# Optimization experiments

Measured on AMD Instinct MI355X. Metric: run time of the kernel, lower is better.

## Reference

```python
import jax, jax.numpy as jnp
import numpy as np

B, N, D = 8, 4096, 2048
DL = 64
NCLS = 2


def setup_inputs() -> dict:
    key = jax.random.key(0)
    k_x, k_tn, k_v, k_w, k_fw, k_fb = jax.random.split(key, 6)
    x = jax.random.normal(k_x, (B, N, D), dtype=jnp.float32)
    # valid patch counts in [1, N] so no bag is fully masked
    true_num = jax.random.randint(k_tn, (B,), 1, N + 1, dtype=jnp.int32)
    std1 = 1.0 / np.sqrt(DL * D)
    V = jax.random.uniform(k_v, (D, DL), minval=-std1, maxval=std1, dtype=jnp.float32)
    std2 = 1.0 / np.sqrt(DL)
    W = jax.random.uniform(k_w, (DL, 1), minval=-std2, maxval=std2, dtype=jnp.float32)
    lim = 1.0 / np.sqrt(D)  # nn.Linear default init
    fc_w = jax.random.uniform(k_fw, (NCLS, D), minval=-lim, maxval=lim, dtype=jnp.float32)
    fc_b = jax.random.uniform(k_fb, (NCLS,), minval=-lim, maxval=lim, dtype=jnp.float32)
    return {"x": x, "true_num": true_num, "V": V, "W": W, "fc_w": fc_w, "fc_b": fc_b}


def reference(x, true_num, V, W, fc_w, fc_b):
    # MILAtten: attention scores over N patches
    x_ = jnp.tanh(jnp.einsum("bnd,dl->bnl", x, V))            # B x N x dl
    dis = jnp.einsum("bnl,lo->bn", x_, W) / np.sqrt(DL)        # B x N
    mask = jnp.arange(x.shape[1])[None, :] < true_num[:, None]  # B x N valid mask
    dis = jnp.where(mask, dis, jnp.float32(-1e20))
    soft_assign = jax.nn.softmax(dis, axis=1)                  # B x N
    feat_fusion = jnp.einsum("bn,bnd->bd", soft_assign, x)     # B x D
    # eval mode: dropout is identity
    logits = feat_fusion @ fc_w.T + fc_b                       # B x class_num
    cls_probs = jax.nn.softmax(logits, axis=1)
    return (cls_probs, soft_assign)
```

## Files before the change

kernel.cpp:

```cpp
#include <hip/hip_runtime.h>
#include <hip/hip_bf16.h>
#include <math.h>

#define BB 8
#define NN 4096
#define DD 2048
#define DLL 64
#define NCLS 2

typedef __attribute__((ext_vector_type(8))) short bf16x8;
typedef __attribute__((ext_vector_type(4))) float f32x4;

__device__ __forceinline__ short f2bf(float f) {
    unsigned int u = __float_as_uint(f);
    unsigned int r = (u + 0x7fffu + ((u >> 16) & 1u)) >> 16;
    return (short)r;
}
__device__ __forceinline__ float bf2f(short s) {
    return __uint_as_float(((unsigned int)(unsigned short)s) << 16);
}

__global__ __launch_bounds__(256) void k_cvt_v(const float* __restrict__ V,
                                               short* __restrict__ Vt) {
    int e = blockIdx.x * 256 + threadIdx.x;
    int k = e >> 6, l = e & 63;
    Vt[(size_t)l * DD + k] = f2bf(V[e]);
}

__global__ __launch_bounds__(256, 2) void k_fused(
        const float* __restrict__ x, const int* __restrict__ tn_p,
        const short* __restrict__ Vt, const float* __restrict__ W,
        float* __restrict__ dis, float* __restrict__ mblk,
        float* __restrict__ lblk, float* __restrict__ partial,
        float* __restrict__ dpart, float* __restrict__ erow_g) {
    __shared__ short Xs[16 * 2048];

    const int tid = threadIdx.x;
    const int blk = blockIdx.x;
    const int b  = blk >> 8;
    const int n0 = (blk & 255) << 4;
    const int tn = tn_p[b];
    if (n0 >= tn) return;

    const float4* xsrc = (const float4*)(x + ((size_t)(b * NN + n0)) * DD);
    #pragma unroll 8
    for (int i = 0; i < 32; i++) {
        int e = tid + (i << 8);
        int row = e >> 9, f4 = e & 511;
        float4 v = xsrc[(size_t)row * 512 + f4];
        int c = f4 >> 1, h = f4 & 1;
        int sc = c ^ (row & 7);
        short4 s;
        s.x = f2bf(v.x); s.y = f2bf(v.y); s.z = f2bf(v.z); s.w = f2bf(v.w);
        *(short4*)&Xs[row * 2048 + sc * 8 + h * 4] = s;
    }
    __syncthreads();

    const int lane = tid & 63, w = tid >> 6;
    const int mm = lane & 15, q = lane >> 4;
    const short* brow = Vt + (size_t)(w * 16 + mm) * DD + q * 8;
    const int arowbase = mm * 2048;
    const int msw = mm & 7;
    f32x4 acc = {0.f, 0.f, 0.f, 0.f};
    #pragma unroll 4
    for (int kc = 0; kc < 64; kc++) {
        int c = kc * 4 + q;
        bf16x8 a  = *(const bf16x8*)&Xs[arowbase + ((c ^ msw) << 3)];
        bf16x8 bv = *(const bf16x8*)(brow + kc * 32);
        acc = __builtin_amdgcn_mfma_f32_16x16x32_bf16(a, bv, acc, 0, 0, 0);
    }

    const float wl = W[w * 16 + mm];
    float* dpb = dpart + blk * 64;
    #pragma unroll
    for (int r = 0; r < 4; r++) {
        float p = tanhf(acc[r]) * wl;
        p += __shfl_xor(p, 1, 64);
        p += __shfl_xor(p, 2, 64);
        p += __shfl_xor(p, 4, 64);
        p += __shfl_xor(p, 8, 64);
        if (mm == 0) dpb[w * 16 + q * 4 + r] = p;
    }
    __syncthreads();

    if (w == 0) {
        float d = (dpb[mm] + dpb[16 + mm] + dpb[32 + mm] + dpb[48 + mm]) * 0.125f;
        int n = n0 + mm;
        if (n >= tn) d = -1e20f;
        if (lane < 16) dis[b * NN + n] = d;
        float mx = d;
        mx = fmaxf(mx, __shfl_xor(mx, 1, 64));
        mx = fmaxf(mx, __shfl_xor(mx, 2, 64));
        mx = fmaxf(mx, __shfl_xor(mx, 4, 64));
        mx = fmaxf(mx, __shfl_xor(mx, 8, 64));
        float e = expf(d - mx);
        float ls = e;
        ls += __shfl_xor(ls, 1, 64);
        ls += __shfl_xor(ls, 2, 64);
        ls += __shfl_xor(ls, 4, 64);
        ls += __shfl_xor(ls, 8, 64);
        if (lane < 16) erow_g[blk * 16 + lane] = e;
        if (lane == 0) { mblk[blk] = mx; lblk[blk] = ls; }
    }
    __syncthreads();

    float er[16];
    const float* eg = erow_g + blk * 16;
    #pragma unroll
    for (int r = 0; r < 16; r++) er[r] = eg[r];

    float facc[8];
    #pragma unroll
    for (int u = 0; u < 8; u++) facc[u] = 0.f;
    #pragma unroll
    for (int r = 0; r < 16; r++) {
        bf16x8 sv = *(const bf16x8*)&Xs[r * 2048 + ((tid ^ (r & 7)) << 3)];
        float e = er[r];
        #pragma unroll
        for (int u = 0; u < 8; u++) facc[u] = fmaf(e, bf2f(sv[u]), facc[u]);
    }
    float* pdst = partial + (size_t)blk * DD + tid * 8;
    float4 o0 = {facc[0], facc[1], facc[2], facc[3]};
    float4 o1 = {facc[4], facc[5], facc[6], facc[7]};
    *(float4*)pdst = o0;
    *(float4*)(pdst + 4) = o1;
}

__global__ __launch_bounds__(256) void k_ml(const int* __restrict__ tn_p,
        const float* __restrict__ mblk, const float* __restrict__ lblk,
        float* __restrict__ alpha, float* __restrict__ MbA,
        float* __restrict__ iLbA) {
    __shared__ float red[4];
    __shared__ float bc;
    const int b = blockIdx.x, t = threadIdx.x;
    const int nvb = (tn_p[b] + 15) >> 4;
    const float mt = (t < nvb) ? mblk[b * 256 + t] : -3.4e38f;
    float mx = mt;
    #pragma unroll
    for (int o = 32; o >= 1; o >>= 1) mx = fmaxf(mx, __shfl_xor(mx, o, 64));
    if ((t & 63) == 0) red[t >> 6] = mx;
    __syncthreads();
    if (t == 0) bc = fmaxf(fmaxf(red[0], red[1]), fmaxf(red[2], red[3]));
    __syncthreads();
    const float M = bc;
    const float sc = (t < nvb) ? expf(mt - M) : 0.f;
    float ls = (t < nvb) ? sc * lblk[b * 256 + t] : 0.f;
    #pragma unroll
    for (int o = 32; o >= 1; o >>= 1) ls += __shfl_xor(ls, o, 64);
    __syncthreads();
    if ((t & 63) == 0) red[t >> 6] = ls;
    __syncthreads();
    if (t == 0) bc = red[0] + red[1] + red[2] + red[3];
    __syncthreads();
    const float L = bc;
    if (t < nvb) alpha[b * 256 + t] = sc / L;
    if (t == 0) { MbA[b] = M; iLbA[b] = 1.f / L; }
}

__global__ __launch_bounds__(256) void k_soft(const float* __restrict__ dis,
        const int* __restrict__ tn_p, const float* __restrict__ MbA,
        const float* __restrict__ iLbA, float* __restrict__ soft) {
    int e = blockIdx.x * 256 + threadIdx.x;
    int b = e >> 10;
    int n = (e & 1023) * 4;
    int tn = tn_p[b];
    float M = MbA[b], iL = iLbA[b];
    float4 dv = ((const float4*)dis)[e];
    float4 o;
    o.x = (n + 0 < tn) ? expf(dv.x - M) * iL : 0.f;
    o.y = (n + 1 < tn) ? expf(dv.y - M) * iL : 0.f;
    o.z = (n + 2 < tn) ? expf(dv.z - M) * iL : 0.f;
    o.w = (n + 3 < tn) ? expf(dv.w - M) * iL : 0.f;
    ((float4*)soft)[e] = o;
}

__global__ __launch_bounds__(256) void k_feat(const int* __restrict__ tn_p,
        const float* __restrict__ alpha, const float* __restrict__ partial,
        float* __restrict__ feat) {
    const int b = blockIdx.x >> 3, s = blockIdx.x & 7, t = threadIdx.x;
    const int nvb = (tn_p[b] + 15) >> 4;
    const int d = s * 256 + t;
    const float* ap = alpha + b * 256;
    const float* pp = partial + ((size_t)b * 256) * DD + d;
    float f = 0.f;
    int i = 0;
    for (; i + 4 <= nvb; i += 4) {
        float f0 = ap[i]     * pp[(size_t)i * DD];
        float f1 = ap[i + 1] * pp[(size_t)(i + 1) * DD];
        float f2 = ap[i + 2] * pp[(size_t)(i + 2) * DD];
        float f3 = ap[i + 3] * pp[(size_t)(i + 3) * DD];
        f += f0 + f1 + f2 + f3;
    }
    for (; i < nvb; i++) f += ap[i] * pp[(size_t)i * DD];
    feat[(size_t)b * DD + d] = f;
}

__global__ __launch_bounds__(256) void k_cls(const float* __restrict__ feat,
        const float* __restrict__ fc_w, const float* __restrict__ fc_b,
        float* __restrict__ cls) {
    __shared__ float red0[4], red1[4];
    const int b = blockIdx.x, t = threadIdx.x;
    const float4* fv = (const float4*)(feat + (size_t)b * DD);
    float4 f0 = fv[t], f1 = fv[t + 256];
    const float4 w00 = ((const float4*)fc_w)[t];
    const float4 w01 = ((const float4*)fc_w)[t + 256];
    const float4 w10 = ((const float4*)(fc_w + DD))[t];
    const float4 w11 = ((const float4*)(fc_w + DD))[t + 256];
    float l0 = f0.x * w00.x + f0.y * w00.y + f0.z * w00.z + f0.w * w00.w +
               f1.x * w01.x + f1.y * w01.y + f1.z * w01.z + f1.w * w01.w;
    float l1 = f0.x * w10.x + f0.y * w10.y + f0.z * w10.z + f0.w * w10.w +
               f1.x * w11.x + f1.y * w11.y + f1.z * w11.z + f1.w * w11.w;
    #pragma unroll
    for (int o = 32; o >= 1; o >>= 1) {
        l0 += __shfl_xor(l0, o, 64);
        l1 += __shfl_xor(l1, o, 64);
    }
    if ((t & 63) == 0) { red0[t >> 6] = l0; red1[t >> 6] = l1; }
    __syncthreads();
    if (t == 0) {
        float L0 = red0[0] + red0[1] + red0[2] + red0[3] + fc_b[0];
        float L1 = red1[0] + red1[1] + red1[2] + red1[3] + fc_b[1];
        float mm = fmaxf(L0, L1);
        float e0 = expf(L0 - mm), e1 = expf(L1 - mm);
        float inv = 1.f / (e0 + e1);
        cls[b * 2 + 0] = e0 * inv;
        cls[b * 2 + 1] = e1 * inv;
    }
}

extern "C" void kernel_launch(void* const* d_in, const int* in_sizes, int n_in,
                              void* d_out, int out_size, void* d_ws, size_t ws_size,
                              hipStream_t stream) {
    (void)in_sizes; (void)n_in; (void)out_size; (void)ws_size;
    const float* x        = (const float*)d_in[0];
    const int*   true_num = (const int*)d_in[1];
    const float* V        = (const float*)d_in[2];
    const float* W        = (const float*)d_in[3];
    const float* fc_w     = (const float*)d_in[4];
    const float* fc_b     = (const float*)d_in[5];

    float* out  = (float*)d_out;
    float* cls  = out;
    float* soft = out + BB * NCLS;

    float* dis     = (float*)d_ws;
    float* mblk    = dis + BB * NN;
    float* lblk    = mblk + 2048;
    float* alpha   = lblk + 2048;
    float* MbA     = alpha + 2048;
    float* iLbA    = MbA + 8;
    float* feat    = iLbA + 8;
    float* dpart   = feat + BB * DD;
    float* erow    = dpart + 2048 * 64;
    float* partial = erow + 2048 * 16;
    short* Vt      = (short*)(partial + (size_t)2048 * DD);

    k_cvt_v<<<512, 256, 0, stream>>>(V, Vt);
    k_fused<<<2048, 256, 0, stream>>>(x, true_num, Vt, W, dis, mblk, lblk,
                                      partial, dpart, erow);
    k_ml<<<BB, 256, 0, stream>>>(true_num, mblk, lblk, alpha, MbA, iLbA);
    k_soft<<<32, 256, 0, stream>>>(dis, true_num, MbA, iLbA, soft);
    k_feat<<<64, 256, 0, stream>>>(true_num, alpha, partial, feat);
    k_cls<<<BB, 256, 0, stream>>>(feat, fc_w, fc_b, cls);
}
```

Measured before the change: 412.9 us.

## Fold classifier projection into fused kernel and collapse tail kernels

Uses linearity to project each block's weighted partial feature sum onto the two classifier rows inside the fused kernel. Only two scalars per block are accumulated atomically, so the 16 MB partial buffer write and the separate feature-reduction pass are gone. The softmax-normalisation, soft-assign and classifier kernels are merged into a single per-batch final kernel. V is also pre-packed into the MFMA fragment order so each lane's B-operand loads are contiguous. The atomics and the per-block fc_w reads are small, but the final kernel runs on only 8 blocks.

```diff
diff --git a/kernel.cpp b/kernel.cpp
--- a/kernel.cpp
+++ b/kernel.cpp
@@ -1,12 +1,9 @@
 #include <hip/hip_runtime.h>
-#include <hip/hip_bf16.h>
 #include <math.h>
 
 #define BB 8
 #define NN 4096
 #define DD 2048
-#define DLL 64
-#define NCLS 2
 
 typedef __attribute__((ext_vector_type(8))) short bf16x8;
 typedef __attribute__((ext_vector_type(4))) float f32x4;
@@ -20,18 +17,26 @@
     return __uint_as_float(((unsigned int)(unsigned short)s) << 16);
 }
 
-__global__ __launch_bounds__(256) void k_cvt_v(const float* __restrict__ V,
-                                               short* __restrict__ Vt) {
+__global__ __launch_bounds__(256) void k_pack_v(const float* __restrict__ V,
+                                                short* __restrict__ Vp,
+                                                float* __restrict__ qblk) {
     int e = blockIdx.x * 256 + threadIdx.x;
-    int k = e >> 6, l = e & 63;
-    Vt[(size_t)l * DD + k] = f2bf(V[e]);
+    if (e < 4096) qblk[e] = 0.f;
+    int lane = e & 63, kc = (e >> 6) & 63, w = e >> 12;
+    int q = lane >> 4, mm = lane & 15;
+    int kb = kc * 32 + q * 8, l = w * 16 + mm;
+    bf16x8 o;
+    #pragma unroll
+    for (int j = 0; j < 8; j++) o[j] = f2bf(V[(size_t)(kb + j) * 64 + l]);
+    *(bf16x8*)(Vp + (size_t)e * 8) = o;
 }
 
 __global__ __launch_bounds__(256, 2) void k_fused(
         const float* __restrict__ x, const int* __restrict__ tn_p,
-        const short* __restrict__ Vt, const float* __restrict__ W,
+        const short* __restrict__ Vp, const float* __restrict__ W,
+        const float* __restrict__ fc_w,
         float* __restrict__ dis, float* __restrict__ mblk,
-        float* __restrict__ lblk, float* __restrict__ partial,
+        float* __restrict__ lblk, float* __restrict__ qblk,
         float* __restrict__ dpart, float* __restrict__ erow_g) {
     __shared__ short Xs[16 * 2048];
 
@@ -58,15 +63,14 @@
 
     const int lane = tid & 63, w = tid >> 6;
     const int mm = lane & 15, q = lane >> 4;
-    const short* brow = Vt + (size_t)(w * 16 + mm) * DD + q * 8;
-    const int arowbase = mm * 2048;
+    const short* vp = Vp + (size_t)w * 32768 + lane * 8;
+    const int arow = mm * 2048;
     const int msw = mm & 7;
     f32x4 acc = {0.f, 0.f, 0.f, 0.f};
     #pragma unroll 4
     for (int kc = 0; kc < 64; kc++) {
-        int c = kc * 4 + q;
-        bf16x8 a  = *(const bf16x8*)&Xs[arowbase + ((c ^ msw) << 3)];
-        bf16x8 bv = *(const bf16x8*)(brow + kc * 32);
+        bf16x8 a  = *(const bf16x8*)&Xs[arow + (((kc * 4 + q) ^ msw) << 3)];
+        bf16x8 bv = *(const bf16x8*)(vp + kc * 512);
         acc = __builtin_amdgcn_mfma_f32_16x16x32_bf16(a, bv, acc, 0, 0, 0);
     }
 
@@ -119,22 +123,37 @@
         #pragma unroll
         for (int u = 0; u < 8; u++) facc[u] = fmaf(e, bf2f(sv[u]), facc[u]);
     }
-    float* pdst = partial + (size_t)blk * DD + tid * 8;
-    float4 o0 = {facc[0], facc[1], facc[2], facc[3]};
-    float4 o1 = {facc[4], facc[5], facc[6], facc[7]};
-    *(float4*)pdst = o0;
-    *(float4*)(pdst + 4) = o1;
-}
-
-__global__ __launch_bounds__(256) void k_ml(const int* __restrict__ tn_p,
+    const float4* w0p = (const float4*)fc_w + tid * 2;
+    const float4* w1p = (const float4*)(fc_w + DD) + tid * 2;
+    float4 wa = w0p[0], wb = w0p[1], wc = w1p[0], wd = w1p[1];
+    float q0 = facc[0] * wa.x + facc[1] * wa.y + facc[2] * wa.z + facc[3] * wa.w +
+               facc[4] * wb.x + facc[5] * wb.y + facc[6] * wb.z + facc[7] * wb.w;
+    float q1 = facc[0] * wc.x + facc[1] * wc.y + facc[2] * wc.z + facc[3] * wc.w +
+               facc[4] * wd.x + facc[5] * wd.y + facc[6] * wd.z + facc[7] * wd.w;
+    #pragma unroll
+    for (int o = 32; o >= 1; o >>= 1) {
+        q0 += __shfl_xor(q0, o, 64);
+        q1 += __shfl_xor(q1, o, 64);
+    }
+    if (lane == 0) {
+        atomicAdd(&qblk[blk * 2 + 0], q0);
+        atomicAdd(&qblk[blk * 2 + 1], q1);
+    }
+}
+
+__global__ __launch_bounds__(256) void k_final(
+        const float* __restrict__ dis, const int* __restrict__ tn_p,
         const float* __restrict__ mblk, const float* __restrict__ lblk,
-        float* __restrict__ alpha, float* __restrict__ MbA,
-        float* __restrict__ iLbA) {
+        const float* __restrict__ qblk, const float* __restrict__ fc_b,
+        float* __restrict__ soft, float* __restrict__ cls) {
     __shared__ float red[4];
+    __shared__ float r3[3][4];
     __shared__ float bc;
     const int b = blockIdx.x, t = threadIdx.x;
-    const int nvb = (tn_p[b] + 15) >> 4;
-    const float mt = (t < nvb) ? mblk[b * 256 + t] : -3.4e38f;
+    const int tn = tn_p[b];
+    const int nvb = (tn + 15) >> 4;
+
+    float mt = (t < nvb) ? mblk[b * 256 + t] : -3.4e38f;
     float mx = mt;
     #pragma unroll
     for (int o = 32; o >= 1; o >>= 1) mx = fmaxf(mx, __shfl_xor(mx, o, 64));
@@ -143,88 +162,51 @@
     if (t == 0) bc = fmaxf(fmaxf(red[0], red[1]), fmaxf(red[2], red[3]));
     __syncthreads();
     const float M = bc;
-    const float sc = (t < nvb) ? expf(mt - M) : 0.f;
+
+    float sc = (t < nvb) ? expf(mt - M) : 0.f;
     float ls = (t < nvb) ? sc * lblk[b * 256 + t] : 0.f;
-    #pragma unroll
-    for (int o = 32; o >= 1; o >>= 1) ls += __shfl_xor(ls, o, 64);
-    __syncthreads();
-    if ((t & 63) == 0) red[t >> 6] = ls;
-    __syncthreads();
-    if (t == 0) bc = red[0] + red[1] + red[2] + red[3];
-    __syncthreads();
-    const float L = bc;
-    if (t < nvb) alpha[b * 256 + t] = sc / L;
-    if (t == 0) { MbA[b] = M; iLbA[b] = 1.f / L; }
-}
-
-__global__ __launch_bounds__(256) void k_soft(const float* __restrict__ dis,
-        const int* __restrict__ tn_p, const float* __restrict__ MbA,
-        const float* __restrict__ iLbA, float* __restrict__ soft) {
-    int e = blockIdx.x * 256 + threadIdx.x;
-    int b = e >> 10;
-    int n = (e & 1023) * 4;
-    int tn = tn_p[b];
-    float M = MbA[b], iL = iLbA[b];
-    float4 dv = ((const float4*)dis)[e];
-    float4 o;
-    o.x = (n + 0 < tn) ? expf(dv.x - M) * iL : 0.f;
-    o.y = (n + 1 < tn) ? expf(dv.y - M) * iL : 0.f;
-    o.z = (n + 2 < tn) ? expf(dv.z - M) * iL : 0.f;
-    o.w = (n + 3 < tn) ? expf(dv.w - M) * iL : 0.f;
-    ((float4*)soft)[e] = o;
-}
-
-__global__ __launch_bounds__(256) void k_feat(const int* __restrict__ tn_p,
-        const float* __restrict__ alpha, const float* __restrict__ partial,
-        float* __restrict__ feat) {
-    const int b = blockIdx.x >> 3, s = blockIdx.x & 7, t = threadIdx.x;
-    const int nvb = (tn_p[b] + 15) >> 4;
-    const int d = s * 256 + t;
-    const float* ap = alpha + b * 256;
-    const float* pp = partial + ((size_t)b * 256) * DD + d;
-    float f = 0.f;
-    int i = 0;
-    for (; i + 4 <= nvb; i += 4) {
-        float f0 = ap[i]     * pp[(size_t)i * DD];
-        float f1 = ap[i + 1] * pp[(size_t)(i + 1) * DD];
-        float f2 = ap[i + 2] * pp[(size_t)(i + 2) * DD];
-        float f3 = ap[i + 3] * pp[(size_t)(i + 3) * DD];
-        f += f0 + f1 + f2 + f3;
-    }
-    for (; i < nvb; i++) f += ap[i] * pp[(size_t)i * DD];
-    feat[(size_t)b * DD + d] = f;
-}
-
-__global__ __launch_bounds__(256) void k_cls(const float* __restrict__ feat,
-        const float* __restrict__ fc_w, const float* __restrict__ fc_b,
-        float* __restrict__ cls) {
-    __shared__ float red0[4], red1[4];
-    const int b = blockIdx.x, t = threadIdx.x;
-    const float4* fv = (const float4*)(feat + (size_t)b * DD);
-    float4 f0 = fv[t], f1 = fv[t + 256];
-    const float4 w00 = ((const float4*)fc_w)[t];
-    const float4 w01 = ((const float4*)fc_w)[t + 256];
-    const float4 w10 = ((const float4*)(fc_w + DD))[t];
-    const float4 w11 = ((const float4*)(fc_w + DD))[t + 256];
-    float l0 = f0.x * w00.x + f0.y * w00.y + f0.z * w00.z + f0.w * w00.w +
-               f1.x * w01.x + f1.y * w01.y + f1.z * w01.z + f1.w * w01.w;
-    float l1 = f0.x * w10.x + f0.y * w10.y + f0.z * w10.z + f0.w * w10.w +
-               f1.x * w11.x + f1.y * w11.y + f1.z * w11.z + f1.w * w11.w;
+    float l0 = 0.f, l1 = 0.f;
+    if (t < nvb) {
+        l0 = sc * qblk[(b * 256 + t) * 2 + 0];
+        l1 = sc * qblk[(b * 256 + t) * 2 + 1];
+    }
     #pragma unroll
     for (int o = 32; o >= 1; o >>= 1) {
+        ls += __shfl_xor(ls, o, 64);
         l0 += __shfl_xor(l0, o, 64);
         l1 += __shfl_xor(l1, o, 64);
     }
-    if ((t & 63) == 0) { red0[t >> 6] = l0; red1[t >> 6] = l1; }
+    if ((t & 63) == 0) {
+        r3[0][t >> 6] = ls; r3[1][t >> 6] = l0; r3[2][t >> 6] = l1;
+    }
     __syncthreads();
     if (t == 0) {
-        float L0 = red0[0] + red0[1] + red0[2] + red0[3] + fc_b[0];
-        float L1 = red1[0] + red1[1] + red1[2] + red1[3] + fc_b[1];
-        float mm = fmaxf(L0, L1);
-        float e0 = expf(L0 - mm), e1 = expf(L1 - mm);
+        float L  = r3[0][0] + r3[0][1] + r3[0][2] + r3[0][3];
+        float Q0 = r3[1][0] + r3[1][1] + r3[1][2] + r3[1][3];
+        float Q1 = r3[2][0] + r3[2][1] + r3[2][2] + r3[2][3];
+        float L0 = Q0 / L + fc_b[0];
+        float L1 = Q1 / L + fc_b[1];
+        float mm2 = fmaxf(L0, L1);
+        float e0 = expf(L0 - mm2), e1 = expf(L1 - mm2);
         float inv = 1.f / (e0 + e1);
         cls[b * 2 + 0] = e0 * inv;
         cls[b * 2 + 1] = e1 * inv;
+        bc = 1.f / L;
+    }
+    __syncthreads();
+    const float iL = bc;
+
+    const float4* dv4 = (const float4*)(dis + (size_t)b * NN);
+    float4* sv4 = (float4*)(soft + (size_t)b * NN);
+    for (int i = t; i < NN / 4; i += 256) {
+        int n = i * 4;
+        float4 dv = dv4[i];
+        float4 o;
+        o.x = (n + 0 < tn) ? expf(dv.x - M) * iL : 0.f;
+        o.y = (n + 1 < tn) ? expf(dv.y - M) * iL : 0.f;
+        o.z = (n + 2 < tn) ? expf(dv.z - M) * iL : 0.f;
+        o.w = (n + 3 < tn) ? expf(dv.w - M) * iL : 0.f;
+        sv4[i] = o;
     }
 }
 
@@ -241,25 +223,19 @@
 
     float* out  = (float*)d_out;
     float* cls  = out;
-    float* soft = out + BB * NCLS;
-
-    float* dis     = (float*)d_ws;
-    float* mblk    = dis + BB * NN;
-    float* lblk    = mblk + 2048;
-    float* alpha   = lblk + 2048;
-    float* MbA     = alpha + 2048;
-    float* iLbA    = MbA + 8;
-    float* feat    = iLbA + 8;
-    float* dpart   = feat + BB * DD;
-    float* erow    = dpart + 2048 * 64;
-    float* partial = erow + 2048 * 16;
-    short* Vt      = (short*)(partial + (size_t)2048 * DD);
-
-    k_cvt_v<<<512, 256, 0, stream>>>(V, Vt);
-    k_fused<<<2048, 256, 0, stream>>>(x, true_num, Vt, W, dis, mblk, lblk,
-                                      partial, dpart, erow);
-    k_ml<<<BB, 256, 0, stream>>>(true_num, mblk, lblk, alpha, MbA, iLbA);
-    k_soft<<<32, 256, 0, stream>>>(dis, true_num, MbA, iLbA, soft);
-    k_feat<<<64, 256, 0, stream>>>(true_num, alpha, partial, feat);
-    k_cls<<<BB, 256, 0, stream>>>(feat, fc_w, fc_b, cls);
-}
+    float* soft = out + BB * 2;
+
+    float* dis   = (float*)d_ws;
+    float* mblk  = dis + (size_t)BB * NN;
+    float* lblk  = mblk + 2048;
+    float* qblk  = lblk + 2048;
+    float* dpart = qblk + 4096;
+    float* erow  = dpart + (size_t)2048 * 64;
+    short* Vp    = (short*)(erow + (size_t)2048 * 16);
+
+    k_pack_v<<<64, 256, 0, stream>>>(V, Vp, qblk);
+    k_fused<<<2048, 256, 0, stream>>>(x, true_num, Vp, W, fc_w,
+                                      dis, mblk, lblk, qblk, dpart, erow);
+    k_final<<<BB, 256, 0, stream>>>(dis, true_num, mblk, lblk, qblk, fc_b,
+                                    soft, cls);
+}
```

Measured after the change: 359.2 us. 1.15x faster.
